# Kernel tuning notes

Measured on AMD Instinct MI355X. Metric: run time of the kernel, lower is better.

The kernel has to match this reference:

```python
import jax, jax.numpy as jnp
import numpy as np

B, L, D, H = 8, 1024, 512, 8  # L must equal len_ for the skew trick
DH = D // H


def setup_inputs() -> dict:
    key = jax.random.key(0)
    ks = jax.random.split(key, 6)
    s = 0.02
    return {
        "x": jax.random.normal(ks[0], (B, L, D), dtype=jnp.float32),
        "Wq": jax.random.normal(ks[1], (D, D), dtype=jnp.float32) * s,
        "Wk": jax.random.normal(ks[2], (D, D), dtype=jnp.float32) * s,
        "Wv": jax.random.normal(ks[3], (D, D), dtype=jnp.float32) * s,
        "We": jax.random.normal(ks[4], (L, DH), dtype=jnp.float32) * s,  # e_projection weight: (len_, d_head)
        "Wo": jax.random.normal(ks[5], (D, D), dtype=jnp.float32) * s,
        "bo": jnp.zeros((D,), dtype=jnp.float32),
        "unused": 0,
    }


def reference(x, Wq, Wk, Wv, We, Wo, bo, unused):
    Bx, Lx, Dx = x.shape
    q = (x @ Wq.T).reshape(Bx, Lx, H, DH)  # blhd
    k = (x @ Wk.T).reshape(Bx, Lx, H, DH)
    v = (x @ Wv.T).reshape(Bx, Lx, H, DH)

    # relative-position logits: e_projection(q) then permute -> (B, H, L, len_)
    qe = jnp.einsum('blhd,ed->bhle', q, We)

    # 'skew' trick: reflect-pad right by L-1, zero-pad (right 1, bottom L-1),
    # reshape (B,H,2L-1,2L) -> (B,H,2L,2L-1), slice [:L, L-1:] -> (B,H,L,L)
    qe = jnp.pad(qe, ((0, 0), (0, 0), (0, 0), (0, Lx - 1)), mode='reflect')
    qe = jnp.pad(qe, ((0, 0), (0, 0), (0, Lx - 1), (0, 1)))
    qe = qe.reshape(Bx, H, 2 * Lx, 2 * Lx - 1)
    s_rel = qe[:, :, :Lx, Lx - 1:]

    scale = 1.0 / jnp.sqrt(jnp.asarray(DH, dtype=x.dtype))
    scores = jnp.einsum('blhd,bshd->bhls', q, k)
    A = jax.nn.softmax(scale * (scores + s_rel), axis=-1)
    V = jnp.einsum('bhls,bshd->blhd', A, v).reshape(Bx, Lx, Dx)
    return V @ Wo.T + bo
```

## Files before the change

### kernel.cpp

```cpp
#include <hip/hip_runtime.h>

#define Lc 1024
#define Dc 512
#define Hc 8
#define DHc 64

typedef __attribute__((ext_vector_type(8))) short bf16x8;
typedef __attribute__((ext_vector_type(4))) float f32x4;
typedef __attribute__((ext_vector_type(16))) float f32x16;

typedef __attribute__((address_space(1))) const unsigned int guint;
typedef __attribute__((address_space(3))) unsigned int luint;

__device__ __forceinline__ void gload_lds16(const void* g, void* l) {
    __builtin_amdgcn_global_load_lds((guint*)g, (luint*)l, 16, 0, 0);
}

__device__ __forceinline__ unsigned short f2bf(float f) {
    unsigned u = __float_as_uint(f);
    u += 0x7fffu + ((u >> 16) & 1u);
    return (unsigned short)(u >> 16);
}
__device__ __forceinline__ unsigned pk2(float a, float b) {
    return (unsigned)f2bf(a) | ((unsigned)f2bf(b) << 16);
}
__device__ __forceinline__ unsigned pk2t(float a, float b) {
    return __builtin_amdgcn_perm(__float_as_uint(b), __float_as_uint(a), 0x07060302u);
}
__device__ __forceinline__ float bf2f(unsigned short s) { return __uint_as_float(((unsigned)s) << 16); }

__device__ __forceinline__ void pl32swap(unsigned &a, unsigned &b) {
    asm volatile("v_permlane32_swap_b32 %0, %1" : "+v"(a), "+v"(b));
}

__global__ void cvt_all_kernel(
    const float* __restrict__ x,  const float* __restrict__ Wq,
    const float* __restrict__ Wk, const float* __restrict__ Wv,
    const float* __restrict__ Wo, const float* __restrict__ We,
    unsigned short* __restrict__ xb,  unsigned short* __restrict__ wqb,
    unsigned short* __restrict__ wkb, unsigned short* __restrict__ wvb,
    unsigned short* __restrict__ wob, unsigned short* __restrict__ wet)
{
    int bid = blockIdx.x;
    const float* src; unsigned short* dst; size_t base;
    if      (bid < 2048) { src = x;  dst = xb;  base = (size_t)bid * 2048; }
    else if (bid < 2176) { src = Wq; dst = wqb; base = (size_t)(bid-2048) * 2048; }
    else if (bid < 2304) { src = Wk; dst = wkb; base = (size_t)(bid-2176) * 2048; }
    else if (bid < 2432) { src = Wv; dst = wvb; base = (size_t)(bid-2304) * 2048; }
    else if (bid < 2560) { src = Wo; dst = wob; base = (size_t)(bid-2432) * 2048; }
    else                 { src = We; dst = wet; base = (size_t)(bid-2560) * 2048; }
    size_t i = base + (size_t)threadIdx.x * 8;
    float4 a = *(const float4*)&src[i];
    float4 b = *(const float4*)&src[i + 4];
    uint4 o = make_uint4(pk2(a.x, a.y), pk2(a.z, a.w), pk2(b.x, b.y), pk2(b.z, b.w));
    *(uint4*)&dst[i] = o;
}

__global__ __launch_bounds__(256, 3) void proj_mfma_kernel(
    const unsigned short* __restrict__ xb,
    const unsigned short* __restrict__ wq, const unsigned short* __restrict__ wk,
    const unsigned short* __restrict__ wv,
    unsigned short* __restrict__ qo, unsigned short* __restrict__ ko,
    unsigned short* __restrict__ vtg, float qscale)
{
    const unsigned short* W;
    if (blockIdx.z == 0)      W = wq;
    else if (blockIdx.z == 1) W = wk;
    else                      W = wv;

    __shared__ unsigned short smem[128 * 136];
    unsigned short* As = smem;
    unsigned short* Bs = smem + 8192;

    const int t = threadIdx.x;
    const int lane = t & 63, w = t >> 6;
    const int lq = lane >> 4, ln = lane & 15;
    const int m0 = blockIdx.y * 128, n0 = blockIdx.x * 128;
    const int wm = (w & 1) * 64, wn = (w >> 1) * 64;
    const int srow = t >> 3;
    const int lsg  = ((t & 7) ^ ((t >> 3) & 7)) * 8;
    const int key  = ln & 7;

    f32x4 acc[4][4];
    #pragma unroll
    for (int i = 0; i < 4; i++)
        #pragma unroll
        for (int j = 0; j < 4; j++) acc[i][j] = (f32x4){0.f,0.f,0.f,0.f};

    for (int c0 = 0; c0 < 512; c0 += 64) {
        __syncthreads();
        #pragma unroll
        for (int g = 0; g < 4; g++) {
            gload_lds16(&xb[(size_t)(m0 + 32*g + srow) * 512 + c0 + lsg], &As[(32*g + srow)*64 + (t&7)*8]);
            gload_lds16(&W [(size_t)(n0 + 32*g + srow) * 512 + c0 + lsg], &Bs[(32*g + srow)*64 + (t&7)*8]);
        }
        __syncthreads();

        #pragma unroll
        for (int kk = 0; kk < 2; kk++) {
            bf16x8 af[4], bf[4];
            #pragma unroll
            for (int i = 0; i < 4; i++)
                af[i] = *(bf16x8*)&As[(wm + 16*i + ln)*64 + ((kk*4 + lq) ^ key)*8];
            #pragma unroll
            for (int j = 0; j < 4; j++)
                bf[j] = *(bf16x8*)&Bs[(wn + 16*j + ln)*64 + ((kk*4 + lq) ^ key)*8];
            #pragma unroll
            for (int i = 0; i < 4; i++)
                #pragma unroll
                for (int j = 0; j < 4; j++)
                    acc[i][j] = __builtin_amdgcn_mfma_f32_16x16x32_bf16(af[i], bf[j], acc[i][j], 0, 0, 0);
        }
    }

    if (blockIdx.z < 2) {
        unsigned short* out = (blockIdx.z == 0) ? qo : ko;
        const float osc = (blockIdx.z == 0) ? qscale : 1.0f;
        #pragma unroll
        for (int i = 0; i < 4; i++) {
            #pragma unroll
            for (int r = 0; r < 4; r++) {
                int m = m0 + wm + 16*i + 4*lq + r;
                int b = m >> 10, l = m & 1023;
                #pragma unroll
                for (int j = 0; j < 4; j++) {
                    int n = n0 + wn + 16*j + ln;
                    int h = n >> 6, dh = n & 63;
                    out[((size_t)((b*Hc + h)*Lc + l))*DHc + dh] = f2bf(acc[i][j][r] * osc);
                }
            }
        }
    } else {
        __syncthreads();
        unsigned short* Ts = smem;
        #pragma unroll
        for (int i = 0; i < 4; i++) {
            int mlb = wm + 16*i + 4*lq;
            #pragma unroll
            for (int j = 0; j < 4; j++) {
                int nl = wn + 16*j + ln;
                *(uint2*)&Ts[nl*136 + mlb] = make_uint2(pk2(acc[i][j][0], acc[i][j][1]),
                                                        pk2(acc[i][j][2], acc[i][j][3]));
            }
        }
        __syncthreads();
        const int b = m0 >> 10, l0m = m0 & 1023;
        const int nl = t >> 1, seg = (t & 1) * 64;
        const int ng = n0 + nl, h = ng >> 6, dh = ng & 63;
        unsigned short* dst = vtg + (((size_t)(b*Hc + h))*DHc + dh)*Lc + l0m + seg;
        #pragma unroll
        for (int u = 0; u < 8; u++)
            *(uint4*)&dst[8*u] = *(uint4*)&Ts[nl*136 + seg + 8*u];
    }
}

__global__ __launch_bounds__(256, 2) void out_mfma_kernel(
    const unsigned short* __restrict__ A, const unsigned short* __restrict__ W,
    const float* __restrict__ bias, float* __restrict__ out)
{
    __shared__ unsigned short As[128 * 64];
    __shared__ unsigned short Bs[64 * 64];

    const int t = threadIdx.x;
    const int lane = t & 63, w = t >> 6;
    const int lq = lane >> 4, ln = lane & 15;
    const int m0 = blockIdx.y * 128, n0 = blockIdx.x * 64;
    const int wm = (w & 1) * 64, wn = (w >> 1) * 32;
    const int srow = t >> 3;
    const int lsg  = ((t & 7) ^ ((t >> 3) & 7)) * 8;
    const int key  = ln & 7;

    f32x4 acc[4][2];
    #pragma unroll
    for (int i = 0; i < 4; i++)
        #pragma unroll
        for (int j = 0; j < 2; j++) acc[i][j] = (f32x4){0.f,0.f,0.f,0.f};

    for (int c0 = 0; c0 < 512; c0 += 64) {
        __syncthreads();
        #pragma unroll
        for (int g = 0; g < 4; g++)
            gload_lds16(&A[(size_t)(m0 + 32*g + srow) * 512 + c0 + lsg], &As[(32*g + srow)*64 + (t&7)*8]);
        #pragma unroll
        for (int g = 0; g < 2; g++)
            gload_lds16(&W[(size_t)(n0 + 32*g + srow) * 512 + c0 + lsg], &Bs[(32*g + srow)*64 + (t&7)*8]);
        __syncthreads();

        #pragma unroll
        for (int kk = 0; kk < 2; kk++) {
            bf16x8 af[4], bf[2];
            #pragma unroll
            for (int i = 0; i < 4; i++)
                af[i] = *(bf16x8*)&As[(wm + 16*i + ln)*64 + ((kk*4 + lq) ^ key)*8];
            #pragma unroll
            for (int j = 0; j < 2; j++)
                bf[j] = *(bf16x8*)&Bs[(wn + 16*j + ln)*64 + ((kk*4 + lq) ^ key)*8];
            #pragma unroll
            for (int i = 0; i < 4; i++)
                #pragma unroll
                for (int j = 0; j < 2; j++)
                    acc[i][j] = __builtin_amdgcn_mfma_f32_16x16x32_bf16(af[i], bf[j], acc[i][j], 0, 0, 0);
        }
    }

    float bb[2];
    #pragma unroll
    for (int j = 0; j < 2; j++) bb[j] = bias[n0 + wn + 16*j + ln];

    #pragma unroll
    for (int i = 0; i < 4; i++) {
        #pragma unroll
        for (int r = 0; r < 4; r++) {
            int m = m0 + wm + 16*i + 4*lq + r;
            #pragma unroll
            for (int j = 0; j < 2; j++) {
                int n = n0 + wn + 16*j + ln;
                out[(size_t)m * Dc + n] = acc[i][j][r] + bb[j];
            }
        }
    }
}

__global__ __launch_bounds__(256, 4) void attn_v12_kernel(
    const unsigned short* __restrict__ q, const unsigned short* __restrict__ k,
    const unsigned short* __restrict__ vtg, const unsigned short* __restrict__ wet,
    unsigned short* __restrict__ attn)
{
    __shared__ unsigned short smem[20480];
    unsigned short* ksp  = smem;
    unsigned short* vtp  = smem + 4096;
    unsigned short* wesp = smem + 8192;
    unsigned short* qes  = smem + 12288;

    const int t    = threadIdx.x;
    const int lane = t & 63, w = t >> 6;
    const int ln31 = lane & 31, hi = lane >> 5;
    const int si   = w >> 1;
    const int li   = w & 1;

    const int n   = blockIdx.x;
    const int xcd = n & 7, idx = n >> 3;
    const int bh  = xcd * 8 + (idx >> 4);
    const int l0  = (idx & 15) * 64;

    const unsigned short* qb  = q   + (size_t)bh * (Lc * DHc);
    const unsigned short* kb  = k   + (size_t)bh * (Lc * DHc);
    const unsigned short* vtb = vtg + (size_t)bh * (DHc * Lc);

    const int srow2 = t >> 3;
    const int lsg2  = ((t & 7) ^ ((t >> 3) & 7)) * 8;
    const int k7    = ln31 & 7;
    const int lloc  = 32*li + ln31;

    bf16x8 qf[4];
    #pragma unroll
    for (int kk = 0; kk < 4; kk++)
        qf[kk] = *(const bf16x8*)&qb[(size_t)(l0 + lloc)*64 + kk*16 + hi*8];

    const int pb0 = 15 - (l0 >> 6);

    gload_lds16(&wet[(size_t)(64*pb0 + srow2)*64 + lsg2],        &vtp [t*8]);
    gload_lds16(&wet[(size_t)(64*pb0 + 32 + srow2)*64 + lsg2],   &vtp [2048 + t*8]);
    gload_lds16(&wet[(size_t)(64*(pb0+1) + srow2)*64 + lsg2],    &wesp[t*8]);
    gload_lds16(&wet[(size_t)(64*(pb0+1) + 32 + srow2)*64 + lsg2], &wesp[2048 + t*8]);
    gload_lds16(&kb [(size_t)srow2*64 + lsg2],                   &ksp [t*8]);
    gload_lds16(&kb [(size_t)(32 + srow2)*64 + lsg2],            &ksp [2048 + t*8]);
    __syncthreads();

    {
        f32x16 qec = (f32x16){0.f,0.f,0.f,0.f,0.f,0.f,0.f,0.f,0.f,0.f,0.f,0.f,0.f,0.f,0.f,0.f};
        #pragma unroll
        for (int kk = 0; kk < 4; kk++) {
            bf16x8 wf = *(bf16x8*)&vtp[(32*si + ln31)*64 + ((2*kk + hi) ^ k7)*8];
            qec = __builtin_amdgcn_mfma_f32_32x32x16_bf16(qf[kk], wf, qec, 0, 0, 0);
        }
        const int rs = ((pb0 & 1)*64 + 32*si + ln31) * 64;
        #pragma unroll
        for (int g = 0; g < 4; g++) {
            const int col = (32*li + 8*g + 4*hi) ^ ((ln31 & 15) << 2);
            *(uint2*)&qes[rs + col] = make_uint2(pk2(qec[4*g], qec[4*g+1]),
                                                 pk2(qec[4*g+2], qec[4*g+3]));
        }
    }

    f32x16 Ov[2];
    #pragma unroll
    for (int dt = 0; dt < 2; dt++)
        Ov[dt] = (f32x16){0.f,0.f,0.f,0.f,0.f,0.f,0.f,0.f,0.f,0.f,0.f,0.f,0.f,0.f,0.f,0.f};
    float Lacc = 0.f;

    int pbOld = pb0 - 1;

    #pragma unroll 1
    for (int s0 = 0; s0 < Lc; s0 += 64) {
        const int c0  = l0 - s0;
        const int ac0 = c0 < 0 ? -c0 : c0;
        const int pb  = (960 - ac0) >> 6;
        const int newp = (pb > pbOld) ? pb + 1 : pb;
        pbOld = pb;
        const int cb = (newp & 1) * 64;
        const bool more = (s0 < Lc - 64);
        const int nc  = c0 - 64;
        const int nac = nc < 0 ? -nc : nc;
        const int npb = (960 - nac) >> 6;
        const int nnp = (npb > pb) ? npb + 1 : npb;

        __syncthreads();

        gload_lds16(&vtb[(size_t)srow2*1024 + s0 + lsg2],        &vtp[t*8]);
        gload_lds16(&vtb[(size_t)(32 + srow2)*1024 + s0 + lsg2], &vtp[2048 + t*8]);

        {
            f32x16 qec = (f32x16){0.f,0.f,0.f,0.f,0.f,0.f,0.f,0.f,0.f,0.f,0.f,0.f,0.f,0.f,0.f,0.f};
            #pragma unroll
            for (int kk = 0; kk < 4; kk++) {
                bf16x8 wf = *(bf16x8*)&wesp[(32*si + ln31)*64 + ((2*kk + hi) ^ k7)*8];
                qec = __builtin_amdgcn_mfma_f32_32x32x16_bf16(qf[kk], wf, qec, 0, 0, 0);
            }
            const int rs = (cb + 32*si + ln31) * 64;
            #pragma unroll
            for (int g = 0; g < 4; g++) {
                const int col = (32*li + 8*g + 4*hi) ^ ((ln31 & 15) << 2);
                *(uint2*)&qes[rs + col] = make_uint2(pk2(qec[4*g], qec[4*g+1]),
                                                     pk2(qec[4*g+2], qec[4*g+3]));
            }
        }

        __syncthreads();

        if (more) {
            gload_lds16(&wet[(size_t)(64*nnp + srow2)*64 + lsg2],      &wesp[t*8]);
            gload_lds16(&wet[(size_t)(64*nnp + 32 + srow2)*64 + lsg2], &wesp[2048 + t*8]);
        }

        f32x16 sc = (f32x16){0.f,0.f,0.f,0.f,0.f,0.f,0.f,0.f,0.f,0.f,0.f,0.f,0.f,0.f,0.f,0.f};
        #pragma unroll
        for (int kk = 0; kk < 4; kk++) {
            bf16x8 kf = *(bf16x8*)&ksp[(32*si + ln31)*64 + ((2*kk + hi) ^ k7)*8];
            sc = __builtin_amdgcn_mfma_f32_32x32x16_bf16(kf, qf[kk], sc, 0, 0, 0);
        }

        float p[16];
        #pragma unroll
        for (int g = 0; g < 4; g++) {
            const int sb = 32*si + 8*g + 4*hi;
            #pragma unroll
            for (int r = 0; r < 4; r++) {
                int d  = c0 + lloc - sb - r;
                int ad = d < 0 ? -d : d;
                int m  = 1023 - ad;
                float bias = bf2f(qes[(m & 127)*64 + (lloc ^ ((m & 15) << 2))]);
                p[4*g + r] = __builtin_amdgcn_exp2f(sc[4*g + r] + bias);
            }
        }
        {
            float t0 = (p[0]+p[1]) + (p[2]+p[3]);
            float t1 = (p[4]+p[5]) + (p[6]+p[7]);
            float t2 = (p[8]+p[9]) + (p[10]+p[11]);
            float t3 = (p[12]+p[13]) + (p[14]+p[15]);
            Lacc += (t0 + t1) + (t2 + t3);
        }
        unsigned d0[4], d1[4];
        #pragma unroll
        for (int g = 0; g < 4; g++) {
            d0[g] = pk2t(p[4*g],     p[4*g + 1]);
            d1[g] = pk2t(p[4*g + 2], p[4*g + 3]);
        }
        bf16x8 pfr[2];
        #pragma unroll
        for (int kk = 0; kk < 2; kk++) {
            pl32swap(d0[2*kk], d0[2*kk + 1]);
            pl32swap(d1[2*kk], d1[2*kk + 1]);
            uint4 fu = make_uint4(d0[2*kk], d1[2*kk], d0[2*kk + 1], d1[2*kk + 1]);
            pfr[kk] = *(bf16x8*)&fu;
        }

        __syncthreads();

        if (more) {
            gload_lds16(&kb[(size_t)(s0 + 64 + srow2)*64 + lsg2],      &ksp[t*8]);
            gload_lds16(&kb[(size_t)(s0 + 64 + 32 + srow2)*64 + lsg2], &ksp[2048 + t*8]);
        }

        #pragma unroll
        for (int kk = 0; kk < 2; kk++)
            #pragma unroll
            for (int dt = 0; dt < 2; dt++) {
                bf16x8 vf = *(bf16x8*)&vtp[(32*dt + ln31)*64 + (((4*si + 2*kk + hi) ^ k7))*8];
                Ov[dt] = __builtin_amdgcn_mfma_f32_32x32x16_bf16(vf, pfr[kk], Ov[dt], 0, 0, 0);
            }
    }

    unsigned la = __float_as_uint(Lacc), lb = la;
    pl32swap(la, lb);
    float Lh = Lacc + __uint_as_float(hi ? la : lb);

    __syncthreads();
    float* scr = (float*)smem;
    if (si == 1) {
        #pragma unroll
        for (int dt = 0; dt < 2; dt++)
            #pragma unroll
            for (int rg = 0; rg < 16; rg++)
                scr[(dt*16 + rg)*128 + li*64 + lane] = Ov[dt][rg];
        scr[32*128 + li*64 + lane] = Lh;
    }
    __syncthreads();
    if (si == 0) {
        const float Lt = Lh + scr[32*128 + li*64 + lane];
        const float inv = 1.f / Lt;
        const int b = bh >> 3, h = bh & 7;
        const int lg = l0 + lloc;
        unsigned short* dst = attn + ((size_t)(b*Lc + lg))*Dc + h*DHc;
        #pragma unroll
        for (int dt = 0; dt < 2; dt++)
            #pragma unroll
            for (int g = 0; g < 4; g++) {
                float v0 = (Ov[dt][4*g]   + scr[(dt*16 + 4*g)*128 + li*64 + lane]) * inv;
                float v1 = (Ov[dt][4*g+1] + scr[(dt*16 + 4*g+1)*128 + li*64 + lane]) * inv;
                float v2 = (Ov[dt][4*g+2] + scr[(dt*16 + 4*g+2)*128 + li*64 + lane]) * inv;
                float v3 = (Ov[dt][4*g+3] + scr[(dt*16 + 4*g+3)*128 + li*64 + lane]) * inv;
                *(uint2*)&dst[32*dt + 8*g + 4*hi] = make_uint2(pk2(v0, v1), pk2(v2, v3));
            }
    }
}

extern "C" void kernel_launch(void* const* d_in, const int* in_sizes, int n_in,
                              void* d_out, int out_size, void* d_ws, size_t ws_size,
                              hipStream_t stream)
{
    (void)in_sizes; (void)n_in; (void)out_size; (void)ws_size;
    const float* x  = (const float*)d_in[0];
    const float* Wq = (const float*)d_in[1];
    const float* Wk = (const float*)d_in[2];
    const float* Wv = (const float*)d_in[3];
    const float* We = (const float*)d_in[4];
    const float* Wo = (const float*)d_in[5];
    const float* bo = (const float*)d_in[6];

    const size_t NT = (size_t)8 * Hc * Lc * DHc;
    unsigned short* qw  = (unsigned short*)d_ws;
    unsigned short* kw  = qw  + NT;
    unsigned short* vtg = kw  + NT;
    unsigned short* xbf = vtg + NT;
    unsigned short* awb = xbf + NT;
    unsigned short* wqb = awb + NT;
    unsigned short* wkb = wqb + 262144;
    unsigned short* wvb = wkb + 262144;
    unsigned short* wob = wvb + 262144;
    unsigned short* wet = wob + 262144;

    cvt_all_kernel<<<2592, 256, 0, stream>>>(x, Wq, Wk, Wv, Wo, We,
                                             xbf, wqb, wkb, wvb, wob, wet);
    proj_mfma_kernel<<<dim3(4, 64, 3), 256, 0, stream>>>(xbf, wqb, wkb, wvb,
                                                         qw, kw, vtg,
                                                         0.125f * 1.44269504089f);
    attn_v12_kernel<<<1024, 256, 0, stream>>>(qw, kw, vtg, wet, awb);
    out_mfma_kernel<<<dim3(8, 64), 256, 0, stream>>>(awb, wob, bo, (float*)d_out);
}
```

Before: 167.1 us.

## Transpose relative-bias LDS layout and gather bias via vector loads with alignbit

Result: faster. 162.6 us (-2.7%).

```diff
diff --git a/kernel.cpp b/kernel.cpp
--- a/kernel.cpp
+++ b/kernel.cpp
@@ -31,6 +31,11 @@
 
 __device__ __forceinline__ void pl32swap(unsigned &a, unsigned &b) {
     asm volatile("v_permlane32_swap_b32 %0, %1" : "+v"(a), "+v"(b));
+}
+__device__ __forceinline__ unsigned alignbit(unsigned hi, unsigned lo, unsigned sh) {
+    unsigned d;
+    asm("v_alignbit_b32 %0, %1, %2, %3" : "=v"(d) : "v"(hi), "v"(lo), "v"(sh));
+    return d;
 }
 
 __global__ void cvt_all_kernel(
@@ -221,7 +226,7 @@
     }
 }
 
-__global__ __launch_bounds__(256, 4) void attn_v12_kernel(
+__global__ __launch_bounds__(256, 4) void attn_v13_kernel(
     const unsigned short* __restrict__ q, const unsigned short* __restrict__ k,
     const unsigned short* __restrict__ vtg, const unsigned short* __restrict__ wet,
     unsigned short* __restrict__ attn)
@@ -251,6 +256,8 @@
     const int lsg2  = ((t & 7) ^ ((t >> 3) & 7)) * 8;
     const int k7    = ln31 & 7;
     const int lloc  = 32*li + ln31;
+    const int wkey  = (lloc & 15) << 2;
+    unsigned short* qrow = &qes[lloc * 128];
 
     bf16x8 qf[4];
     #pragma unroll
@@ -272,14 +279,14 @@
         #pragma unroll
         for (int kk = 0; kk < 4; kk++) {
             bf16x8 wf = *(bf16x8*)&vtp[(32*si + ln31)*64 + ((2*kk + hi) ^ k7)*8];
-            qec = __builtin_amdgcn_mfma_f32_32x32x16_bf16(qf[kk], wf, qec, 0, 0, 0);
-        }
-        const int rs = ((pb0 & 1)*64 + 32*si + ln31) * 64;
+            qec = __builtin_amdgcn_mfma_f32_32x32x16_bf16(wf, qf[kk], qec, 0, 0, 0);
+        }
+        const int cb = (pb0 & 1) * 64;
         #pragma unroll
         for (int g = 0; g < 4; g++) {
-            const int col = (32*li + 8*g + 4*hi) ^ ((ln31 & 15) << 2);
-            *(uint2*)&qes[rs + col] = make_uint2(pk2(qec[4*g], qec[4*g+1]),
-                                                 pk2(qec[4*g+2], qec[4*g+3]));
+            const int col = (cb + 32*si + 8*g + 4*hi) ^ wkey;
+            *(uint2*)&qrow[col] = make_uint2(pk2(qec[4*g], qec[4*g+1]),
+                                             pk2(qec[4*g+2], qec[4*g+3]));
         }
     }
 
@@ -315,14 +322,13 @@
             #pragma unroll
             for (int kk = 0; kk < 4; kk++) {
                 bf16x8 wf = *(bf16x8*)&wesp[(32*si + ln31)*64 + ((2*kk + hi) ^ k7)*8];
-                qec = __builtin_amdgcn_mfma_f32_32x32x16_bf16(qf[kk], wf, qec, 0, 0, 0);
-            }
-            const int rs = (cb + 32*si + ln31) * 64;
+                qec = __builtin_amdgcn_mfma_f32_32x32x16_bf16(wf, qf[kk], qec, 0, 0, 0);
+            }
             #pragma unroll
             for (int g = 0; g < 4; g++) {
-                const int col = (32*li + 8*g + 4*hi) ^ ((ln31 & 15) << 2);
-                *(uint2*)&qes[rs + col] = make_uint2(pk2(qec[4*g], qec[4*g+1]),
-                                                     pk2(qec[4*g+2], qec[4*g+3]));
+                const int col = (cb + 32*si + 8*g + 4*hi) ^ wkey;
+                *(uint2*)&qrow[col] = make_uint2(pk2(qec[4*g], qec[4*g+1]),
+                                                 pk2(qec[4*g+2], qec[4*g+3]));
             }
         }
 
@@ -341,18 +347,56 @@
         }
 
         float p[16];
-        #pragma unroll
-        for (int g = 0; g < 4; g++) {
-            const int sb = 32*si + 8*g + 4*hi;
-            #pragma unroll
-            for (int r = 0; r < 4; r++) {
-                int d  = c0 + lloc - sb - r;
-                int ad = d < 0 ? -d : d;
-                int m  = 1023 - ad;
-                float bias = bf2f(qes[(m & 127)*64 + (lloc ^ ((m & 15) << 2))]);
-                p[4*g + r] = __builtin_amdgcn_exp2f(sc[4*g + r] + bias);
-            }
-        }
+        if (c0 >= 128 || c0 <= -64) {
+            const bool asc = (c0 >= 128);
+            #pragma unroll
+            for (int g = 0; g < 4; g++) {
+                const int dbase0 = c0 + lloc - (32*si + 8*g + 4*hi);
+                const int base = asc ? (1023 - dbase0) : (1020 + dbase0);
+                const int a  = (base & ~3) & 127;
+                const int a2 = (a + 4) & 127;
+                const uint2 w01 = *(const uint2*)&qrow[a  ^ wkey];
+                const uint2 w23 = *(const uint2*)&qrow[a2 ^ wkey];
+                const int off = base & 3;
+                const bool oh = (off >= 2);
+                const unsigned wl = oh ? w01.y : w01.x;
+                const unsigned wm = oh ? w23.x : w01.y;
+                const unsigned wh = oh ? w23.y : w23.x;
+                const unsigned sh = (unsigned)(off & 1) * 16u;
+                const unsigned r0 = alignbit(wm, wl, sh);
+                const unsigned r1 = alignbit(wh, wm, sh);
+                float b0, b1, b2, b3;
+                if (asc) {
+                    b0 = __uint_as_float(r0 << 16);
+                    b1 = __uint_as_float(r0 & 0xffff0000u);
+                    b2 = __uint_as_float(r1 << 16);
+                    b3 = __uint_as_float(r1 & 0xffff0000u);
+                } else {
+                    b0 = __uint_as_float(r1 & 0xffff0000u);
+                    b1 = __uint_as_float(r1 << 16);
+                    b2 = __uint_as_float(r0 & 0xffff0000u);
+                    b3 = __uint_as_float(r0 << 16);
+                }
+                p[4*g+0] = __builtin_amdgcn_exp2f(sc[4*g+0] + b0);
+                p[4*g+1] = __builtin_amdgcn_exp2f(sc[4*g+1] + b1);
+                p[4*g+2] = __builtin_amdgcn_exp2f(sc[4*g+2] + b2);
+                p[4*g+3] = __builtin_amdgcn_exp2f(sc[4*g+3] + b3);
+            }
+        } else {
+            #pragma unroll
+            for (int g = 0; g < 4; g++) {
+                const int sb = 32*si + 8*g + 4*hi;
+                #pragma unroll
+                for (int r = 0; r < 4; r++) {
+                    int d  = c0 + lloc - sb - r;
+                    int ad = d < 0 ? -d : d;
+                    int m  = 1023 - ad;
+                    float bias = bf2f(qrow[(m & 127) ^ wkey]);
+                    p[4*g + r] = __builtin_amdgcn_exp2f(sc[4*g + r] + bias);
+                }
+            }
+        }
+
         {
             float t0 = (p[0]+p[1]) + (p[2]+p[3]);
             float t1 = (p[4]+p[5]) + (p[6]+p[7]);
@@ -455,6 +499,6 @@
     proj_mfma_kernel<<<dim3(4, 64, 3), 256, 0, stream>>>(xbf, wqb, wkb, wvb,
                                                          qw, kw, vtg,
                                                          0.125f * 1.44269504089f);
-    attn_v12_kernel<<<1024, 256, 0, stream>>>(qw, kw, vtg, wet, awb);
+    attn_v13_kernel<<<1024, 256, 0, stream>>>(qw, kw, vtg, wet, awb);
     out_mfma_kernel<<<dim3(8, 64), 256, 0, stream>>>(awb, wob, bo, (float*)d_out);
 }
```
